# Optimization experiments

Hardware: AMD Instinct MI355X
Metric: run time of the kernel (lower is better)

The kernel has to match this reference:

```python
import jax, jax.numpy as jnp
import numpy as np

T = 4096          # tokens (batch*seq)
D = 768           # moe_intermediate_size (token hidden dim)
I = 2048          # intermediate_size (FFN inner dim)
E = 8             # num_experts


def setup_inputs() -> dict:
    key = jax.random.key(0)
    k_x, k_p, k_g, k_u, k_d = jax.random.split(key, 5)
    hidden_states = jax.random.normal(k_x, (T, D), dtype=jnp.float32)
    position_index = jax.random.randint(k_p, (T,), 0, E, dtype=jnp.int64)
    behavior_index = jnp.zeros((T,), dtype=jnp.int64)  # unused (behavior_injection=False)
    s = 0.02
    # torch Linear weight layout: [out_features, in_features]
    gate_w = jax.random.normal(k_g, (E, I, D), dtype=jnp.float32) * s
    up_w = jax.random.normal(k_u, (E, I, D), dtype=jnp.float32) * s
    down_w = jax.random.normal(k_d, (E, D, I), dtype=jnp.float32) * s
    return {
        "hidden_states": hidden_states,
        "position_index": position_index,
        "behavior_index": behavior_index,
        "gate_w": gate_w,
        "up_w": up_w,
        "down_w": down_w,
    }


def reference(hidden_states, position_index, behavior_index, gate_w, up_w, down_w):
    # Sparse MoE dispatch: each token routed to exactly one expert by position_index.
    # Dropout rate is 0.0 (eval) -> identity. behavior_injection=False -> behavior_index unused.
    num_experts = gate_w.shape[0]
    out = jnp.zeros_like(hidden_states)
    for e in range(num_experts):  # structural loop over fixed expert count
        mask = (position_index == e)[:, None]          # [T, 1]
        g = hidden_states @ gate_w[e].T                 # [T, I]
        u = hidden_states @ up_w[e].T                   # [T, I]
        y = (jax.nn.silu(g) * u) @ down_w[e].T          # [T, D]
        out = out + jnp.where(mask, y, 0.0)             # scatter-combine
    return out
```

## Files before the change

kernel.cpp:

```cpp
#include <hip/hip_runtime.h>
#include <hip/hip_bf16.h>

#define T_TOK 4096
#define DDIM  768
#define IDIM  2048
#define NEXP  8

typedef __attribute__((ext_vector_type(8))) short  bfrag;
typedef __attribute__((ext_vector_type(4))) float  ffrag;

static __device__ __forceinline__ unsigned short f2bf(float f) {
    union { float f; unsigned u; } v; v.f = f;
    unsigned r = v.u + 0x7FFFu + ((v.u >> 16) & 1u);
    return (unsigned short)(r >> 16);
}

static __device__ __forceinline__ unsigned cvt2(float x, float y) {
    return (unsigned)f2bf(x) | ((unsigned)f2bf(y) << 16);
}

__global__ void k_sort(const int* __restrict__ pos, int* __restrict__ ws_i,
                       int* __restrict__ perm) {
    __shared__ int hist[NEXP], cursor[NEXP];
    const int tid = threadIdx.x;
    if (tid < NEXP) hist[tid] = 0;
    __syncthreads();
    for (int i = tid; i < T_TOK; i += 1024)
        atomicAdd(&hist[pos[i]], 1);
    __syncthreads();
    if (tid == 0) {
        int s = 0;
        for (int e = 0; e < NEXP; ++e) {
            cursor[e] = s;
            ws_i[e] = hist[e];
            ws_i[16 + e] = s;
            s += hist[e];
        }
        ws_i[16 + NEXP] = s;
    }
    __syncthreads();
    for (int i = tid; i < T_TOK; i += 1024) {
        int p = atomicAdd(&cursor[pos[i]], 1);
        perm[p] = i;
    }
}

__global__ void k_gather(const float* __restrict__ x, const int* __restrict__ perm,
                         unsigned short* __restrict__ xg) {
    int p = blockIdx.x;
    int tok = perm[p];
    int j = threadIdx.x * 4;
    const float4 v = *reinterpret_cast<const float4*>(x + (size_t)tok * DDIM + j);
    uint2 o;
    o.x = cvt2(v.x, v.y);
    o.y = cvt2(v.z, v.w);
    *reinterpret_cast<uint2*>(xg + (size_t)p * DDIM + j) = o;
}

__launch_bounds__(256, 2)
__global__ void k_gemm1(const unsigned short* __restrict__ xg,
                        const float* __restrict__ gate_w,
                        const float* __restrict__ up_w,
                        unsigned short* __restrict__ hg,
                        const int* __restrict__ ws_i) {
    const int e   = blockIdx.z;
    const int cnt = ws_i[e];
    const int m0  = blockIdx.y * 128;
    if (m0 >= cnt) return;
    const int off = ws_i[16 + e];
    const int n0  = blockIdx.x * 64;

    const int tid  = threadIdx.x;
    const int lane = tid & 63;
    const int wave = tid >> 6;
    const int wm   = wave & 1;
    const int wn   = wave >> 1;

    __shared__ __align__(16) unsigned short lsA[128 * 56];
    __shared__ __align__(16) unsigned short lsG[64 * 56];
    __shared__ __align__(16) unsigned short lsU[64 * 56];

    const float* gate_e = gate_w + (size_t)e * (IDIM * DDIM);
    const float* up_e   = up_w   + (size_t)e * (IDIM * DDIM);

    const int ar = tid >> 2;
    const int aq = tid & 3;
    const int br = tid >> 3;
    const int bq = tid & 7;

    int g0 = off + m0 + ar;      if (g0 > T_TOK - 1) g0 = T_TOK - 1;
    int g1 = off + m0 + ar + 64; if (g1 > T_TOK - 1) g1 = T_TOK - 1;
    const unsigned short* a0p = xg + (size_t)g0 * DDIM + aq * 8;
    const unsigned short* a1p = xg + (size_t)g1 * DDIM + aq * 8;
    const float* gp0 = gate_e + (size_t)(n0 + br)      * DDIM + bq * 4;
    const float* gp1 = gate_e + (size_t)(n0 + br + 32) * DDIM + bq * 4;
    const float* up0 = up_e   + (size_t)(n0 + br)      * DDIM + bq * 4;
    const float* up1 = up_e   + (size_t)(n0 + br + 32) * DDIM + bq * 4;

    uint4  pa0 = *reinterpret_cast<const uint4*>(a0p);
    uint4  pa1 = *reinterpret_cast<const uint4*>(a1p);
    float4 pg0 = *reinterpret_cast<const float4*>(gp0);
    float4 pg1 = *reinterpret_cast<const float4*>(gp1);
    float4 pu0 = *reinterpret_cast<const float4*>(up0);
    float4 pu1 = *reinterpret_cast<const float4*>(up1);

    ffrag accG[4][2], accU[4][2];
    const ffrag fz = {0.f, 0.f, 0.f, 0.f};
    for (int mi = 0; mi < 4; ++mi)
        for (int ni = 0; ni < 2; ++ni) { accG[mi][ni] = fz; accU[mi][ni] = fz; }

    const int koff = (lane >> 4) * 8;
    const int rsel = lane & 15;

    for (int kt = 0; kt < DDIM / 32; ++kt) {
        *reinterpret_cast<uint4*>(&lsA[ar * 56 + aq * 8])        = pa0;
        *reinterpret_cast<uint4*>(&lsA[(ar + 64) * 56 + aq * 8]) = pa1;
        { uint2 o; o.x = cvt2(pg0.x, pg0.y); o.y = cvt2(pg0.z, pg0.w);
          *reinterpret_cast<uint2*>(&lsG[br * 56 + bq * 4]) = o; }
        { uint2 o; o.x = cvt2(pg1.x, pg1.y); o.y = cvt2(pg1.z, pg1.w);
          *reinterpret_cast<uint2*>(&lsG[(br + 32) * 56 + bq * 4]) = o; }
        { uint2 o; o.x = cvt2(pu0.x, pu0.y); o.y = cvt2(pu0.z, pu0.w);
          *reinterpret_cast<uint2*>(&lsU[br * 56 + bq * 4]) = o; }
        { uint2 o; o.x = cvt2(pu1.x, pu1.y); o.y = cvt2(pu1.z, pu1.w);
          *reinterpret_cast<uint2*>(&lsU[(br + 32) * 56 + bq * 4]) = o; }
        __syncthreads();

        if (kt < DDIM / 32 - 1) {
            const int kb = (kt + 1) * 32;
            pa0 = *reinterpret_cast<const uint4*>(a0p + kb);
            pa1 = *reinterpret_cast<const uint4*>(a1p + kb);
            pg0 = *reinterpret_cast<const float4*>(gp0 + kb);
            pg1 = *reinterpret_cast<const float4*>(gp1 + kb);
            pu0 = *reinterpret_cast<const float4*>(up0 + kb);
            pu1 = *reinterpret_cast<const float4*>(up1 + kb);
        }

        bfrag a[4], bg[2], bu[2];
        #pragma unroll
        for (int mi = 0; mi < 4; ++mi)
            a[mi] = *reinterpret_cast<const bfrag*>(&lsA[(wm * 64 + mi * 16 + rsel) * 56 + koff]);
        #pragma unroll
        for (int ni = 0; ni < 2; ++ni) {
            bg[ni] = *reinterpret_cast<const bfrag*>(&lsG[(wn * 32 + ni * 16 + rsel) * 56 + koff]);
            bu[ni] = *reinterpret_cast<const bfrag*>(&lsU[(wn * 32 + ni * 16 + rsel) * 56 + koff]);
        }
        #pragma unroll
        for (int mi = 0; mi < 4; ++mi)
            #pragma unroll
            for (int ni = 0; ni < 2; ++ni) {
                accG[mi][ni] = __builtin_amdgcn_mfma_f32_16x16x32_bf16(a[mi], bg[ni], accG[mi][ni], 0, 0, 0);
                accU[mi][ni] = __builtin_amdgcn_mfma_f32_16x16x32_bf16(a[mi], bu[ni], accU[mi][ni], 0, 0, 0);
            }
        __syncthreads();
    }

    const int colb  = lane & 15;
    const int rquad = (lane >> 4) * 4;
    #pragma unroll
    for (int mi = 0; mi < 4; ++mi)
        #pragma unroll
        for (int ni = 0; ni < 2; ++ni) {
            int n = n0 + wn * 32 + ni * 16 + colb;
            #pragma unroll
            for (int r = 0; r < 4; ++r) {
                int ml = wm * 64 + mi * 16 + rquad + r;
                if (m0 + ml < cnt) {
                    float g = accG[mi][ni][r];
                    float u = accU[mi][ni][r];
                    float h = (g / (1.0f + __expf(-g))) * u;
                    hg[(size_t)(off + m0 + ml) * IDIM + n] = f2bf(h);
                }
            }
        }
}

__launch_bounds__(256, 2)
__global__ void k_gemm2(const unsigned short* __restrict__ hg,
                        const float* __restrict__ down_w,
                        float* __restrict__ out,
                        const int* __restrict__ ws_i,
                        const int* __restrict__ perm) {
    const int e     = blockIdx.z & 7;
    const int split = blockIdx.z >> 3;
    const int cnt = ws_i[e];
    const int m0  = blockIdx.y * 128;
    if (m0 >= cnt) return;
    const int off = ws_i[16 + e];
    const int n0  = blockIdx.x * 64;

    const int tid  = threadIdx.x;
    const int lane = tid & 63;
    const int wave = tid >> 6;
    const int wm   = wave & 1;
    const int wn   = wave >> 1;

    __shared__ __align__(16) unsigned short lsA[128 * 56];
    __shared__ __align__(16) unsigned short lsB[64 * 56];

    const float* down_e = down_w + (size_t)e * (DDIM * IDIM);

    const int ar = tid >> 2;
    const int aq = tid & 3;
    const int br = tid >> 3;
    const int bq = tid & 7;

    int g0 = off + m0 + ar;      if (g0 > T_TOK - 1) g0 = T_TOK - 1;
    int g1 = off + m0 + ar + 64; if (g1 > T_TOK - 1) g1 = T_TOK - 1;
    const unsigned short* a0p = hg + (size_t)g0 * IDIM + split * 512 + aq * 8;
    const unsigned short* a1p = hg + (size_t)g1 * IDIM + split * 512 + aq * 8;
    const float* bp0 = down_e + (size_t)(n0 + br)      * IDIM + split * 512 + bq * 4;
    const float* bp1 = down_e + (size_t)(n0 + br + 32) * IDIM + split * 512 + bq * 4;

    uint4  pa0 = *reinterpret_cast<const uint4*>(a0p);
    uint4  pa1 = *reinterpret_cast<const uint4*>(a1p);
    float4 pb0 = *reinterpret_cast<const float4*>(bp0);
    float4 pb1 = *reinterpret_cast<const float4*>(bp1);

    ffrag acc[4][2];
    const ffrag fz = {0.f, 0.f, 0.f, 0.f};
    for (int mi = 0; mi < 4; ++mi)
        for (int ni = 0; ni < 2; ++ni) acc[mi][ni] = fz;

    const int koff = (lane >> 4) * 8;
    const int rsel = lane & 15;

    for (int kt = 0; kt < 16; ++kt) {
        *reinterpret_cast<uint4*>(&lsA[ar * 56 + aq * 8])        = pa0;
        *reinterpret_cast<uint4*>(&lsA[(ar + 64) * 56 + aq * 8]) = pa1;
        { uint2 o; o.x = cvt2(pb0.x, pb0.y); o.y = cvt2(pb0.z, pb0.w);
          *reinterpret_cast<uint2*>(&lsB[br * 56 + bq * 4]) = o; }
        { uint2 o; o.x = cvt2(pb1.x, pb1.y); o.y = cvt2(pb1.z, pb1.w);
          *reinterpret_cast<uint2*>(&lsB[(br + 32) * 56 + bq * 4]) = o; }
        __syncthreads();

        if (kt < 15) {
            const int kb = (kt + 1) * 32;
            pa0 = *reinterpret_cast<const uint4*>(a0p + kb);
            pa1 = *reinterpret_cast<const uint4*>(a1p + kb);
            pb0 = *reinterpret_cast<const float4*>(bp0 + kb);
            pb1 = *reinterpret_cast<const float4*>(bp1 + kb);
        }

        bfrag a[4], b[2];
        #pragma unroll
        for (int mi = 0; mi < 4; ++mi)
            a[mi] = *reinterpret_cast<const bfrag*>(&lsA[(wm * 64 + mi * 16 + rsel) * 56 + koff]);
        #pragma unroll
        for (int ni = 0; ni < 2; ++ni)
            b[ni] = *reinterpret_cast<const bfrag*>(&lsB[(wn * 32 + ni * 16 + rsel) * 56 + koff]);
        #pragma unroll
        for (int mi = 0; mi < 4; ++mi)
            #pragma unroll
            for (int ni = 0; ni < 2; ++ni)
                acc[mi][ni] = __builtin_amdgcn_mfma_f32_16x16x32_bf16(a[mi], b[ni], acc[mi][ni], 0, 0, 0);
        __syncthreads();
    }

    const int colb  = lane & 15;
    const int rquad = (lane >> 4) * 4;
    #pragma unroll
    for (int mi = 0; mi < 4; ++mi)
        #pragma unroll
        for (int ni = 0; ni < 2; ++ni) {
            int n = n0 + wn * 32 + ni * 16 + colb;
            #pragma unroll
            for (int r = 0; r < 4; ++r) {
                int ml = wm * 64 + mi * 16 + rquad + r;
                if (m0 + ml < cnt) {
                    int tok = perm[off + m0 + ml];
                    unsafeAtomicAdd(&out[(size_t)tok * DDIM + n], acc[mi][ni][r]);
                }
            }
        }
}

extern "C" void kernel_launch(void* const* d_in, const int* in_sizes, int n_in,
                              void* d_out, int out_size, void* d_ws, size_t ws_size,
                              hipStream_t stream) {
    const float* x      = (const float*)d_in[0];
    const int*   pos    = (const int*)d_in[1];
    const float* gate_w = (const float*)d_in[3];
    const float* up_w   = (const float*)d_in[4];
    const float* down_w = (const float*)d_in[5];
    float* out = (float*)d_out;

    char* ws = (char*)d_ws;
    int* ws_i = (int*)ws;
    int* perm = (int*)(ws + 1024);
    unsigned short* xg = (unsigned short*)(ws + 32768);
    unsigned short* hg = (unsigned short*)(ws + (8u << 20));

    (void)hipMemsetAsync(d_out, 0, (size_t)out_size * sizeof(float), stream);
    k_sort<<<dim3(1), dim3(1024), 0, stream>>>(pos, ws_i, perm);
    k_gather<<<dim3(T_TOK), dim3(192), 0, stream>>>(x, perm, xg);

    dim3 g1(IDIM / 64, 32, NEXP);
    k_gemm1<<<g1, dim3(256), 0, stream>>>(xg, gate_w, up_w, hg, ws_i);
    dim3 g2(DDIM / 64, 32, NEXP * 4);
    k_gemm2<<<g2, dim3(256), 0, stream>>>(hg, down_w, out, ws_i, perm);
}
```

Baseline: 305.4 us.

## Remove split-K atomics in down GEMM, loop M-tiles, warp-aggregate sort atomics

The down-projection GEMM drops its 4-way split-K and writes output rows with plain stores instead of atomic adds. Because every token goes to exactly one expert, each output row is fully written, so the output memset is also removed. The gate/up GEMM grid shrinks to 2 M-groups per expert that loop over M-tiles, which avoids launching many blocks that exit immediately. The sort kernel uses ballot-based warp aggregation for its histogram and cursor atomics. The trade-off is that the down GEMM now runs fewer blocks, each with a 4x longer K loop, which may leave CUs underused.

```diff
diff --git a/kernel.cpp b/kernel.cpp
--- a/kernel.cpp
+++ b/kernel.cpp
@@ -22,11 +22,19 @@
 __global__ void k_sort(const int* __restrict__ pos, int* __restrict__ ws_i,
                        int* __restrict__ perm) {
     __shared__ int hist[NEXP], cursor[NEXP];
-    const int tid = threadIdx.x;
+    const int tid  = threadIdx.x;
+    const int lane = tid & 63;
     if (tid < NEXP) hist[tid] = 0;
     __syncthreads();
-    for (int i = tid; i < T_TOK; i += 1024)
-        atomicAdd(&hist[pos[i]], 1);
+    for (int i = tid; i < T_TOK; i += 1024) {
+        int e = pos[i];
+        #pragma unroll
+        for (int ee = 0; ee < NEXP; ++ee) {
+            unsigned long long m = __ballot(e == ee);
+            if (e == ee && lane == (__ffsll((long long)m) - 1))
+                atomicAdd(&hist[ee], __popcll(m));
+        }
+    }
     __syncthreads();
     if (tid == 0) {
         int s = 0;
@@ -40,7 +48,20 @@
     }
     __syncthreads();
     for (int i = tid; i < T_TOK; i += 1024) {
-        int p = atomicAdd(&cursor[pos[i]], 1);
+        int e = pos[i];
+        int p = 0;
+        #pragma unroll
+        for (int ee = 0; ee < NEXP; ++ee) {
+            unsigned long long m = __ballot(e == ee);
+            if (e == ee) {
+                int leader = __ffsll((long long)m) - 1;
+                int rank = __popcll(m & ((1ull << lane) - 1ull));
+                int base = 0;
+                if (lane == leader) base = atomicAdd(&cursor[ee], __popcll(m));
+                base = __shfl(base, leader);
+                p = base + rank;
+            }
+        }
         perm[p] = i;
     }
 }
@@ -65,8 +86,10 @@
                         const int* __restrict__ ws_i) {
     const int e   = blockIdx.z;
     const int cnt = ws_i[e];
-    const int m0  = blockIdx.y * 128;
-    if (m0 >= cnt) return;
+    if (cnt == 0) return;
+    const int nmt = (cnt + 127) >> 7;
+    const int mg  = blockIdx.y;
+    if (mg >= nmt) return;
     const int off = ws_i[16 + e];
     const int n0  = blockIdx.x * 64;
 
@@ -88,90 +111,96 @@
     const int br = tid >> 3;
     const int bq = tid & 7;
 
-    int g0 = off + m0 + ar;      if (g0 > T_TOK - 1) g0 = T_TOK - 1;
-    int g1 = off + m0 + ar + 64; if (g1 > T_TOK - 1) g1 = T_TOK - 1;
-    const unsigned short* a0p = xg + (size_t)g0 * DDIM + aq * 8;
-    const unsigned short* a1p = xg + (size_t)g1 * DDIM + aq * 8;
     const float* gp0 = gate_e + (size_t)(n0 + br)      * DDIM + bq * 4;
     const float* gp1 = gate_e + (size_t)(n0 + br + 32) * DDIM + bq * 4;
     const float* up0 = up_e   + (size_t)(n0 + br)      * DDIM + bq * 4;
     const float* up1 = up_e   + (size_t)(n0 + br + 32) * DDIM + bq * 4;
 
-    uint4  pa0 = *reinterpret_cast<const uint4*>(a0p);
-    uint4  pa1 = *reinterpret_cast<const uint4*>(a1p);
-    float4 pg0 = *reinterpret_cast<const float4*>(gp0);
-    float4 pg1 = *reinterpret_cast<const float4*>(gp1);
-    float4 pu0 = *reinterpret_cast<const float4*>(up0);
-    float4 pu1 = *reinterpret_cast<const float4*>(up1);
-
-    ffrag accG[4][2], accU[4][2];
-    const ffrag fz = {0.f, 0.f, 0.f, 0.f};
-    for (int mi = 0; mi < 4; ++mi)
-        for (int ni = 0; ni < 2; ++ni) { accG[mi][ni] = fz; accU[mi][ni] = fz; }
-
     const int koff = (lane >> 4) * 8;
     const int rsel = lane & 15;
-
-    for (int kt = 0; kt < DDIM / 32; ++kt) {
-        *reinterpret_cast<uint4*>(&lsA[ar * 56 + aq * 8])        = pa0;
-        *reinterpret_cast<uint4*>(&lsA[(ar + 64) * 56 + aq * 8]) = pa1;
-        { uint2 o; o.x = cvt2(pg0.x, pg0.y); o.y = cvt2(pg0.z, pg0.w);
-          *reinterpret_cast<uint2*>(&lsG[br * 56 + bq * 4]) = o; }
-        { uint2 o; o.x = cvt2(pg1.x, pg1.y); o.y = cvt2(pg1.z, pg1.w);
-          *reinterpret_cast<uint2*>(&lsG[(br + 32) * 56 + bq * 4]) = o; }
-        { uint2 o; o.x = cvt2(pu0.x, pu0.y); o.y = cvt2(pu0.z, pu0.w);
-          *reinterpret_cast<uint2*>(&lsU[br * 56 + bq * 4]) = o; }
-        { uint2 o; o.x = cvt2(pu1.x, pu1.y); o.y = cvt2(pu1.z, pu1.w);
-          *reinterpret_cast<uint2*>(&lsU[(br + 32) * 56 + bq * 4]) = o; }
-        __syncthreads();
-
-        if (kt < DDIM / 32 - 1) {
-            const int kb = (kt + 1) * 32;
-            pa0 = *reinterpret_cast<const uint4*>(a0p + kb);
-            pa1 = *reinterpret_cast<const uint4*>(a1p + kb);
-            pg0 = *reinterpret_cast<const float4*>(gp0 + kb);
-            pg1 = *reinterpret_cast<const float4*>(gp1 + kb);
-            pu0 = *reinterpret_cast<const float4*>(up0 + kb);
-            pu1 = *reinterpret_cast<const float4*>(up1 + kb);
-        }
-
-        bfrag a[4], bg[2], bu[2];
-        #pragma unroll
-        for (int mi = 0; mi < 4; ++mi)
-            a[mi] = *reinterpret_cast<const bfrag*>(&lsA[(wm * 64 + mi * 16 + rsel) * 56 + koff]);
-        #pragma unroll
-        for (int ni = 0; ni < 2; ++ni) {
-            bg[ni] = *reinterpret_cast<const bfrag*>(&lsG[(wn * 32 + ni * 16 + rsel) * 56 + koff]);
-            bu[ni] = *reinterpret_cast<const bfrag*>(&lsU[(wn * 32 + ni * 16 + rsel) * 56 + koff]);
-        }
-        #pragma unroll
-        for (int mi = 0; mi < 4; ++mi)
-            #pragma unroll
-            for (int ni = 0; ni < 2; ++ni) {
-                accG[mi][ni] = __builtin_amdgcn_mfma_f32_16x16x32_bf16(a[mi], bg[ni], accG[mi][ni], 0, 0, 0);
-                accU[mi][ni] = __builtin_amdgcn_mfma_f32_16x16x32_bf16(a[mi], bu[ni], accU[mi][ni], 0, 0, 0);
-            }
-        __syncthreads();
-    }
-
     const int colb  = lane & 15;
     const int rquad = (lane >> 4) * 4;
-    #pragma unroll
-    for (int mi = 0; mi < 4; ++mi)
-        #pragma unroll
-        for (int ni = 0; ni < 2; ++ni) {
-            int n = n0 + wn * 32 + ni * 16 + colb;
-            #pragma unroll
-            for (int r = 0; r < 4; ++r) {
-                int ml = wm * 64 + mi * 16 + rquad + r;
-                if (m0 + ml < cnt) {
-                    float g = accG[mi][ni][r];
-                    float u = accU[mi][ni][r];
-                    float h = (g / (1.0f + __expf(-g))) * u;
-                    hg[(size_t)(off + m0 + ml) * IDIM + n] = f2bf(h);
+
+    for (int mt = mg; mt < nmt; mt += 2) {
+        const int m0 = mt * 128;
+        int g0 = off + m0 + ar;      if (g0 > T_TOK - 1) g0 = T_TOK - 1;
+        int g1 = off + m0 + ar + 64; if (g1 > T_TOK - 1) g1 = T_TOK - 1;
+        const unsigned short* a0p = xg + (size_t)g0 * DDIM + aq * 8;
+        const unsigned short* a1p = xg + (size_t)g1 * DDIM + aq * 8;
+
+        uint4  pa0 = *reinterpret_cast<const uint4*>(a0p);
+        uint4  pa1 = *reinterpret_cast<const uint4*>(a1p);
+        float4 pg0 = *reinterpret_cast<const float4*>(gp0);
+        float4 pg1 = *reinterpret_cast<const float4*>(gp1);
+        float4 pu0 = *reinterpret_cast<const float4*>(up0);
+        float4 pu1 = *reinterpret_cast<const float4*>(up1);
+
+        ffrag accG[4][2], accU[4][2];
+        const ffrag fz = {0.f, 0.f, 0.f, 0.f};
+        #pragma unroll
+        for (int mi = 0; mi < 4; ++mi)
+            #pragma unroll
+            for (int ni = 0; ni < 2; ++ni) { accG[mi][ni] = fz; accU[mi][ni] = fz; }
+
+        for (int kt = 0; kt < DDIM / 32; ++kt) {
+            *reinterpret_cast<uint4*>(&lsA[ar * 56 + aq * 8])        = pa0;
+            *reinterpret_cast<uint4*>(&lsA[(ar + 64) * 56 + aq * 8]) = pa1;
+            { uint2 o; o.x = cvt2(pg0.x, pg0.y); o.y = cvt2(pg0.z, pg0.w);
+              *reinterpret_cast<uint2*>(&lsG[br * 56 + bq * 4]) = o; }
+            { uint2 o; o.x = cvt2(pg1.x, pg1.y); o.y = cvt2(pg1.z, pg1.w);
+              *reinterpret_cast<uint2*>(&lsG[(br + 32) * 56 + bq * 4]) = o; }
+            { uint2 o; o.x = cvt2(pu0.x, pu0.y); o.y = cvt2(pu0.z, pu0.w);
+              *reinterpret_cast<uint2*>(&lsU[br * 56 + bq * 4]) = o; }
+            { uint2 o; o.x = cvt2(pu1.x, pu1.y); o.y = cvt2(pu1.z, pu1.w);
+              *reinterpret_cast<uint2*>(&lsU[(br + 32) * 56 + bq * 4]) = o; }
+            __syncthreads();
+
+            if (kt < DDIM / 32 - 1) {
+                const int kb = (kt + 1) * 32;
+                pa0 = *reinterpret_cast<const uint4*>(a0p + kb);
+                pa1 = *reinterpret_cast<const uint4*>(a1p + kb);
+                pg0 = *reinterpret_cast<const float4*>(gp0 + kb);
+                pg1 = *reinterpret_cast<const float4*>(gp1 + kb);
+                pu0 = *reinterpret_cast<const float4*>(up0 + kb);
+                pu1 = *reinterpret_cast<const float4*>(up1 + kb);
+            }
+
+            bfrag a[4], bg[2], bu[2];
+            #pragma unroll
+            for (int mi = 0; mi < 4; ++mi)
+                a[mi] = *reinterpret_cast<const bfrag*>(&lsA[(wm * 64 + mi * 16 + rsel) * 56 + koff]);
+            #pragma unroll
+            for (int ni = 0; ni < 2; ++ni) {
+                bg[ni] = *reinterpret_cast<const bfrag*>(&lsG[(wn * 32 + ni * 16 + rsel) * 56 + koff]);
+                bu[ni] = *reinterpret_cast<const bfrag*>(&lsU[(wn * 32 + ni * 16 + rsel) * 56 + koff]);
+            }
+            #pragma unroll
+            for (int mi = 0; mi < 4; ++mi)
+                #pragma unroll
+                for (int ni = 0; ni < 2; ++ni) {
+                    accG[mi][ni] = __builtin_amdgcn_mfma_f32_16x16x32_bf16(a[mi], bg[ni], accG[mi][ni], 0, 0, 0);
+                    accU[mi][ni] = __builtin_amdgcn_mfma_f32_16x16x32_bf16(a[mi], bu[ni], accU[mi][ni], 0, 0, 0);
                 }
-            }
-        }
+            __syncthreads();
+        }
+
+        #pragma unroll
+        for (int mi = 0; mi < 4; ++mi)
+            #pragma unroll
+            for (int ni = 0; ni < 2; ++ni) {
+                int n = n0 + wn * 32 + ni * 16 + colb;
+                #pragma unroll
+                for (int r = 0; r < 4; ++r) {
+                    int ml = wm * 64 + mi * 16 + rquad + r;
+                    if (m0 + ml < cnt) {
+                        float g = accG[mi][ni][r];
+                        float u = accU[mi][ni][r];
+                        float h = (g / (1.0f + __expf(-g))) * u;
+                        hg[(size_t)(off + m0 + ml) * IDIM + n] = f2bf(h);
+                    }
+                }
+            }
+    }
 }
 
 __launch_bounds__(256, 2)
@@ -180,11 +209,12 @@
                         float* __restrict__ out,
                         const int* __restrict__ ws_i,
                         const int* __restrict__ perm) {
-    const int e     = blockIdx.z & 7;
-    const int split = blockIdx.z >> 3;
+    const int e   = blockIdx.y;
     const int cnt = ws_i[e];
-    const int m0  = blockIdx.y * 128;
-    if (m0 >= cnt) return;
+    if (cnt == 0) return;
+    const int nmt = (cnt + 127) >> 7;
+    const int mg  = blockIdx.z;
+    if (mg >= nmt) return;
     const int off = ws_i[16 + e];
     const int n0  = blockIdx.x * 64;
 
@@ -204,74 +234,78 @@
     const int br = tid >> 3;
     const int bq = tid & 7;
 
-    int g0 = off + m0 + ar;      if (g0 > T_TOK - 1) g0 = T_TOK - 1;
-    int g1 = off + m0 + ar + 64; if (g1 > T_TOK - 1) g1 = T_TOK - 1;
-    const unsigned short* a0p = hg + (size_t)g0 * IDIM + split * 512 + aq * 8;
-    const unsigned short* a1p = hg + (size_t)g1 * IDIM + split * 512 + aq * 8;
-    const float* bp0 = down_e + (size_t)(n0 + br)      * IDIM + split * 512 + bq * 4;
-    const float* bp1 = down_e + (size_t)(n0 + br + 32) * IDIM + split * 512 + bq * 4;
-
-    uint4  pa0 = *reinterpret_cast<const uint4*>(a0p);
-    uint4  pa1 = *reinterpret_cast<const uint4*>(a1p);
-    float4 pb0 = *reinterpret_cast<const float4*>(bp0);
-    float4 pb1 = *reinterpret_cast<const float4*>(bp1);
-
-    ffrag acc[4][2];
-    const ffrag fz = {0.f, 0.f, 0.f, 0.f};
-    for (int mi = 0; mi < 4; ++mi)
-        for (int ni = 0; ni < 2; ++ni) acc[mi][ni] = fz;
+    const float* bp0 = down_e + (size_t)(n0 + br)      * IDIM + bq * 4;
+    const float* bp1 = down_e + (size_t)(n0 + br + 32) * IDIM + bq * 4;
 
     const int koff = (lane >> 4) * 8;
     const int rsel = lane & 15;
-
-    for (int kt = 0; kt < 16; ++kt) {
-        *reinterpret_cast<uint4*>(&lsA[ar * 56 + aq * 8])        = pa0;
-        *reinterpret_cast<uint4*>(&lsA[(ar + 64) * 56 + aq * 8]) = pa1;
-        { uint2 o; o.x = cvt2(pb0.x, pb0.y); o.y = cvt2(pb0.z, pb0.w);
-          *reinterpret_cast<uint2*>(&lsB[br * 56 + bq * 4]) = o; }
-        { uint2 o; o.x = cvt2(pb1.x, pb1.y); o.y = cvt2(pb1.z, pb1.w);
-          *reinterpret_cast<uint2*>(&lsB[(br + 32) * 56 + bq * 4]) = o; }
-        __syncthreads();
-
-        if (kt < 15) {
-            const int kb = (kt + 1) * 32;
-            pa0 = *reinterpret_cast<const uint4*>(a0p + kb);
-            pa1 = *reinterpret_cast<const uint4*>(a1p + kb);
-            pb0 = *reinterpret_cast<const float4*>(bp0 + kb);
-            pb1 = *reinterpret_cast<const float4*>(bp1 + kb);
-        }
-
-        bfrag a[4], b[2];
-        #pragma unroll
-        for (int mi = 0; mi < 4; ++mi)
-            a[mi] = *reinterpret_cast<const bfrag*>(&lsA[(wm * 64 + mi * 16 + rsel) * 56 + koff]);
-        #pragma unroll
-        for (int ni = 0; ni < 2; ++ni)
-            b[ni] = *reinterpret_cast<const bfrag*>(&lsB[(wn * 32 + ni * 16 + rsel) * 56 + koff]);
-        #pragma unroll
-        for (int mi = 0; mi < 4; ++mi)
-            #pragma unroll
-            for (int ni = 0; ni < 2; ++ni)
-                acc[mi][ni] = __builtin_amdgcn_mfma_f32_16x16x32_bf16(a[mi], b[ni], acc[mi][ni], 0, 0, 0);
-        __syncthreads();
-    }
-
     const int colb  = lane & 15;
     const int rquad = (lane >> 4) * 4;
-    #pragma unroll
-    for (int mi = 0; mi < 4; ++mi)
-        #pragma unroll
-        for (int ni = 0; ni < 2; ++ni) {
-            int n = n0 + wn * 32 + ni * 16 + colb;
+
+    for (int mt = mg; mt < nmt; mt += 4) {
+        const int m0 = mt * 128;
+        int g0 = off + m0 + ar;      if (g0 > T_TOK - 1) g0 = T_TOK - 1;
+        int g1 = off + m0 + ar + 64; if (g1 > T_TOK - 1) g1 = T_TOK - 1;
+        const unsigned short* a0p = hg + (size_t)g0 * IDIM + aq * 8;
+        const unsigned short* a1p = hg + (size_t)g1 * IDIM + aq * 8;
+
+        uint4  pa0 = *reinterpret_cast<const uint4*>(a0p);
+        uint4  pa1 = *reinterpret_cast<const uint4*>(a1p);
+        float4 pb0 = *reinterpret_cast<const float4*>(bp0);
+        float4 pb1 = *reinterpret_cast<const float4*>(bp1);
+
+        ffrag acc[4][2];
+        const ffrag fz = {0.f, 0.f, 0.f, 0.f};
+        #pragma unroll
+        for (int mi = 0; mi < 4; ++mi)
+            #pragma unroll
+            for (int ni = 0; ni < 2; ++ni) acc[mi][ni] = fz;
+
+        for (int kt = 0; kt < IDIM / 32; ++kt) {
+            *reinterpret_cast<uint4*>(&lsA[ar * 56 + aq * 8])        = pa0;
+            *reinterpret_cast<uint4*>(&lsA[(ar + 64) * 56 + aq * 8]) = pa1;
+            { uint2 o; o.x = cvt2(pb0.x, pb0.y); o.y = cvt2(pb0.z, pb0.w);
+              *reinterpret_cast<uint2*>(&lsB[br * 56 + bq * 4]) = o; }
+            { uint2 o; o.x = cvt2(pb1.x, pb1.y); o.y = cvt2(pb1.z, pb1.w);
+              *reinterpret_cast<uint2*>(&lsB[(br + 32) * 56 + bq * 4]) = o; }
+            __syncthreads();
+
+            if (kt < IDIM / 32 - 1) {
+                const int kb = (kt + 1) * 32;
+                pa0 = *reinterpret_cast<const uint4*>(a0p + kb);
+                pa1 = *reinterpret_cast<const uint4*>(a1p + kb);
+                pb0 = *reinterpret_cast<const float4*>(bp0 + kb);
+                pb1 = *reinterpret_cast<const float4*>(bp1 + kb);
+            }
+
+            bfrag a[4], b[2];
+            #pragma unroll
+            for (int mi = 0; mi < 4; ++mi)
+                a[mi] = *reinterpret_cast<const bfrag*>(&lsA[(wm * 64 + mi * 16 + rsel) * 56 + koff]);
+            #pragma unroll
+            for (int ni = 0; ni < 2; ++ni)
+                b[ni] = *reinterpret_cast<const bfrag*>(&lsB[(wn * 32 + ni * 16 + rsel) * 56 + koff]);
+            #pragma unroll
+            for (int mi = 0; mi < 4; ++mi)
+                #pragma unroll
+                for (int ni = 0; ni < 2; ++ni)
+                    acc[mi][ni] = __builtin_amdgcn_mfma_f32_16x16x32_bf16(a[mi], b[ni], acc[mi][ni], 0, 0, 0);
+            __syncthreads();
+        }
+
+        #pragma unroll
+        for (int mi = 0; mi < 4; ++mi)
             #pragma unroll
             for (int r = 0; r < 4; ++r) {
                 int ml = wm * 64 + mi * 16 + rquad + r;
                 if (m0 + ml < cnt) {
                     int tok = perm[off + m0 + ml];
-                    unsafeAtomicAdd(&out[(size_t)tok * DDIM + n], acc[mi][ni][r]);
+                    float* orow = out + (size_t)tok * DDIM + n0 + wn * 32 + colb;
+                    orow[0]  = acc[mi][0][r];
+                    orow[16] = acc[mi][1][r];
                 }
             }
-        }
+    }
 }
 
 extern "C" void kernel_launch(void* const* d_in, const int* in_sizes, int n_in,
@@ -290,12 +324,11 @@
     unsigned short* xg = (unsigned short*)(ws + 32768);
     unsigned short* hg = (unsigned short*)(ws + (8u << 20));
 
-    (void)hipMemsetAsync(d_out, 0, (size_t)out_size * sizeof(float), stream);
     k_sort<<<dim3(1), dim3(1024), 0, stream>>>(pos, ws_i, perm);
     k_gather<<<dim3(T_TOK), dim3(192), 0, stream>>>(x, perm, xg);
 
-    dim3 g1(IDIM / 64, 32, NEXP);
+    dim3 g1(IDIM / 64, 2, NEXP);
     k_gemm1<<<g1, dim3(256), 0, stream>>>(xg, gate_w, up_w, hg, ws_i);
-    dim3 g2(DDIM / 64, 32, NEXP * 4);
+    dim3 g2(DDIM / 64, NEXP, 4);
     k_gemm2<<<g2, dim3(256), 0, stream>>>(hg, down_w, out, ws_i, perm);
 }
```

Measured after the change: 346.4 us. +13.4%, slower.
